# Kernel tuning notes

Hardware: AMD Instinct MI355X
Metric: run time of the kernel (lower is better)

Reference implementation:

```python
import jax, jax.numpy as jnp
import numpy as np

N_NODES = 50000
N_EDGES = 800000
D_FEAT = 64
EDGE_DIM = 64


def setup_inputs() -> dict:
    key = jax.random.key(0)
    k1, k2, k3, k4 = jax.random.split(key, 4)
    node_feats = jax.random.normal(k1, (N_NODES, D_FEAT), dtype=jnp.float32)
    senders = jax.random.randint(k2, (N_EDGES,), 0, N_NODES, dtype=jnp.int32)
    receivers = jax.random.randint(k3, (N_EDGES,), 0, N_NODES, dtype=jnp.int32)
    # Dense(edge_dim) applied to concat([recv, send]) of width 2*D_FEAT
    W = jax.random.normal(k4, (2 * D_FEAT, EDGE_DIM), dtype=jnp.float32) / np.sqrt(2.0 * D_FEAT)
    b = jnp.zeros((EDGE_DIM,), dtype=jnp.float32)
    return {"node_feats": node_feats, "senders": senders, "receivers": receivers, "W": W, "b": b}


def reference(node_feats, senders, receivers, W, b):
    # gather node features at each edge endpoint: [E, D]
    feats_send = node_feats[senders]
    feats_recv = node_feats[receivers]
    # concat(recv, send) -> [E, 2D], Dense + tanh -> [E, edge_dim]
    edge_feats = jnp.concatenate([feats_recv, feats_send], axis=-1)
    return jnp.tanh(edge_feats @ W + b)
```

## Files before the change

### kernel.cpp

```cpp
#include <hip/hip_runtime.h>

#define N_EDGES 800000
#define N_NODES 50000
#define D 64

typedef __attribute__((ext_vector_type(8))) short bf16x8;
typedef __attribute__((ext_vector_type(4))) float f32x4;

__device__ __forceinline__ unsigned short f2bf(float f) {
    unsigned int u = __float_as_uint(f);
    u += 0x7fffu + ((u >> 16) & 1u);
    return (unsigned short)(u >> 16);
}
__device__ __forceinline__ unsigned int pack2(float a, float b) {
    return (unsigned int)f2bf(a) | ((unsigned int)f2bf(b) << 16);
}

__global__ __launch_bounds__(256) void prep(
    const float* __restrict__ nf, const float* __restrict__ W,
    unsigned short* __restrict__ nodes_bf, unsigned short* __restrict__ wfrag)
{
    if (blockIdx.x == gridDim.x - 1) {
#pragma unroll
        for (int i = 0; i < 4; ++i) {
            const int idx = i * 256 + threadIdx.x;
            const int ki = idx >> 8;
            const int nt = (idx >> 6) & 3;
            const int l  = idx & 63;
            const int m  = l & 15, q = l >> 4;
            const int kbase = ki * 32 + q * 8;
            const int n = nt * 16 + m;
            unsigned short* dst = wfrag + idx * 8;
#pragma unroll
            for (int j = 0; j < 8; ++j)
                dst[j] = f2bf(W[(kbase + j) * D + n]);
        }
    } else {
        const long base = ((long)blockIdx.x * 256 + threadIdx.x) * 8;
        if (base < (long)N_NODES * D) {
            const float4 lo = *(const float4*)(nf + base);
            const float4 hi = *(const float4*)(nf + base + 4);
            uint4 p;
            p.x = pack2(lo.x, lo.y);
            p.y = pack2(lo.z, lo.w);
            p.z = pack2(hi.x, hi.y);
            p.w = pack2(hi.z, hi.w);
            *(uint4*)(nodes_bf + base) = p;
        }
    }
}

__global__ __launch_bounds__(256) void edge_mlp(
    const unsigned short* __restrict__ nodes_bf,
    const bf16x8*        __restrict__ wfrag,
    const int*   __restrict__ senders,
    const int*   __restrict__ receivers,
    const float* __restrict__ bias,
    float*       __restrict__ out)
{
    __shared__ bf16x8 lds_b[1024];

#pragma unroll
    for (int i = 0; i < 4; ++i) {
        const int idx = i * 256 + threadIdx.x;
        lds_b[idx] = wfrag[idx];
    }
    __syncthreads();

    const int lane = threadIdx.x & 63;
    const int m    = lane & 15;
    const int q    = lane >> 4;
    const long wid = (long)blockIdx.x * 4 + (threadIdx.x >> 6);
    const long e0  = wid * 64;

    const int rv = receivers[e0 + lane];
    const int sv = senders[e0 + lane];
    int nidx[2][4];
#pragma unroll
    for (int mt = 0; mt < 4; ++mt) {
        nidx[0][mt] = __shfl(rv, mt * 16 + m, 64);
        nidx[1][mt] = __shfl(sv, mt * 16 + m, 64);
    }

    f32x4 acc[4][4];
#pragma unroll
    for (int mt = 0; mt < 4; ++mt)
#pragma unroll
        for (int nt = 0; nt < 4; ++nt)
            acc[mt][nt] = (f32x4)0.0f;

#pragma unroll
    for (int ki = 0; ki < 4; ++ki) {
        const int k0 = ki * 32 + q * 8;

        bf16x8 bfrag[4];
#pragma unroll
        for (int nt = 0; nt < 4; ++nt)
            bfrag[nt] = lds_b[(ki * 4 + nt) * 64 + lane];

        bf16x8 afrag[4];
#pragma unroll
        for (int mt = 0; mt < 4; ++mt) {
            const int node = nidx[ki >> 1][mt];
            afrag[mt] = *(const bf16x8*)(nodes_bf + node * D + (k0 & 63));
        }

#pragma unroll
        for (int mt = 0; mt < 4; ++mt)
#pragma unroll
            for (int nt = 0; nt < 4; ++nt)
                acc[mt][nt] = __builtin_amdgcn_mfma_f32_16x16x32_bf16(
                    afrag[mt], bfrag[nt], acc[mt][nt], 0, 0, 0);
    }

    float bv[4];
#pragma unroll
    for (int nt = 0; nt < 4; ++nt) bv[nt] = bias[nt * 16 + m];

#pragma unroll
    for (int mt = 0; mt < 4; ++mt) {
#pragma unroll
        for (int r = 0; r < 4; ++r) {
            const long row = e0 + mt * 16 + q * 4 + r;
            float* op = out + row * D + m;
#pragma unroll
            for (int nt = 0; nt < 4; ++nt) {
                const float x  = acc[mt][nt][r] + bv[nt];
                const float ax = __builtin_fabsf(x);
                const float t  = __expf(-2.0f * ax);
                float y = (1.0f - t) * __builtin_amdgcn_rcpf(1.0f + t);
                y = __builtin_copysignf(y, x);
                __builtin_nontemporal_store(y, op + nt * 16);
            }
        }
    }
}

extern "C" void kernel_launch(void* const* d_in, const int* in_sizes, int n_in,
                              void* d_out, int out_size, void* d_ws, size_t ws_size,
                              hipStream_t stream) {
    const float* node_feats = (const float*)d_in[0];
    const int*   senders    = (const int*)d_in[1];
    const int*   receivers  = (const int*)d_in[2];
    const float* W          = (const float*)d_in[3];
    const float* bias       = (const float*)d_in[4];
    float*       out        = (float*)d_out;

    unsigned short* nodes_bf = (unsigned short*)d_ws;
    unsigned short* wfrag    = (unsigned short*)((char*)d_ws + (size_t)N_NODES * D * 2);

    const int node_blocks = ((N_NODES * D / 8) + 255) / 256;
    prep<<<node_blocks + 1, 256, 0, stream>>>(node_feats, W, nodes_bf, wfrag);

    const int n_blocks = N_EDGES / 256;
    edge_mlp<<<n_blocks, 256, 0, stream>>>(nodes_bf, (const bf16x8*)wfrag,
                                           senders, receivers, bias, out);
}
```

Measured before the change: 257.2 us.

## Shrink per-wave edge tile to 16 edges and raise occupancy

Each wave now handles 16 edges instead of 64, so its accumulator drops from 16 MFMA tiles to 4. All A-fragment gathers are issued up front, and the grid is four times larger. Launch bounds request 5 blocks per SM so more waves are resident to hide gather latency. In exchange, every block reloads the 16KB weight fragment into LDS for a quarter as many edges, adding LDS-fill and sync overhead per edge.

```diff
diff --git a/kernel.cpp b/kernel.cpp
--- a/kernel.cpp
+++ b/kernel.cpp
@@ -50,7 +50,7 @@
     }
 }
 
-__global__ __launch_bounds__(256) void edge_mlp(
+__global__ __launch_bounds__(256, 5) void edge_mlp(
     const unsigned short* __restrict__ nodes_bf,
     const bf16x8*        __restrict__ wfrag,
     const int*   __restrict__ senders,
@@ -71,46 +71,29 @@
     const int m    = lane & 15;
     const int q    = lane >> 4;
     const long wid = (long)blockIdx.x * 4 + (threadIdx.x >> 6);
-    const long e0  = wid * 64;
+    const long e0  = wid * 16;
 
-    const int rv = receivers[e0 + lane];
-    const int sv = senders[e0 + lane];
-    int nidx[2][4];
+    const int nr = receivers[e0 + m];
+    const int ns = senders[e0 + m];
+
+    const unsigned short* rrow = nodes_bf + (long)nr * D + q * 8;
+    const unsigned short* srow = nodes_bf + (long)ns * D + q * 8;
+    bf16x8 afrag[4];
+    afrag[0] = *(const bf16x8*)(rrow);
+    afrag[1] = *(const bf16x8*)(rrow + 32);
+    afrag[2] = *(const bf16x8*)(srow);
+    afrag[3] = *(const bf16x8*)(srow + 32);
+
+    f32x4 acc[4];
 #pragma unroll
-    for (int mt = 0; mt < 4; ++mt) {
-        nidx[0][mt] = __shfl(rv, mt * 16 + m, 64);
-        nidx[1][mt] = __shfl(sv, mt * 16 + m, 64);
-    }
-
-    f32x4 acc[4][4];
-#pragma unroll
-    for (int mt = 0; mt < 4; ++mt)
-#pragma unroll
-        for (int nt = 0; nt < 4; ++nt)
-            acc[mt][nt] = (f32x4)0.0f;
+    for (int nt = 0; nt < 4; ++nt) acc[nt] = (f32x4)0.0f;
 
 #pragma unroll
     for (int ki = 0; ki < 4; ++ki) {
-        const int k0 = ki * 32 + q * 8;
-
-        bf16x8 bfrag[4];
 #pragma unroll
         for (int nt = 0; nt < 4; ++nt)
-            bfrag[nt] = lds_b[(ki * 4 + nt) * 64 + lane];
-
-        bf16x8 afrag[4];
-#pragma unroll
-        for (int mt = 0; mt < 4; ++mt) {
-            const int node = nidx[ki >> 1][mt];
-            afrag[mt] = *(const bf16x8*)(nodes_bf + node * D + (k0 & 63));
-        }
-
-#pragma unroll
-        for (int mt = 0; mt < 4; ++mt)
-#pragma unroll
-            for (int nt = 0; nt < 4; ++nt)
-                acc[mt][nt] = __builtin_amdgcn_mfma_f32_16x16x32_bf16(
-                    afrag[mt], bfrag[nt], acc[mt][nt], 0, 0, 0);
+            acc[nt] = __builtin_amdgcn_mfma_f32_16x16x32_bf16(
+                afrag[ki], lds_b[(ki * 4 + nt) * 64 + lane], acc[nt], 0, 0, 0);
     }
 
     float bv[4];
@@ -118,20 +101,16 @@
     for (int nt = 0; nt < 4; ++nt) bv[nt] = bias[nt * 16 + m];
 
 #pragma unroll
-    for (int mt = 0; mt < 4; ++mt) {
+    for (int r = 0; r < 4; ++r) {
+        float* op = out + (e0 + q * 4 + r) * D + m;
 #pragma unroll
-        for (int r = 0; r < 4; ++r) {
-            const long row = e0 + mt * 16 + q * 4 + r;
-            float* op = out + row * D + m;
-#pragma unroll
-            for (int nt = 0; nt < 4; ++nt) {
-                const float x  = acc[mt][nt][r] + bv[nt];
-                const float ax = __builtin_fabsf(x);
-                const float t  = __expf(-2.0f * ax);
-                float y = (1.0f - t) * __builtin_amdgcn_rcpf(1.0f + t);
-                y = __builtin_copysignf(y, x);
-                __builtin_nontemporal_store(y, op + nt * 16);
-            }
+        for (int nt = 0; nt < 4; ++nt) {
+            const float x  = acc[nt][r] + bv[nt];
+            const float ax = __builtin_fabsf(x);
+            const float t  = __expf(-2.0f * ax);
+            float y = (1.0f - t) * __builtin_amdgcn_rcpf(1.0f + t);
+            y = __builtin_copysignf(y, x);
+            __builtin_nontemporal_store(y, op + nt * 16);
         }
     }
 }
@@ -152,7 +131,7 @@
     const int node_blocks = ((N_NODES * D / 8) + 255) / 256;
     prep<<<node_blocks + 1, 256, 0, stream>>>(node_feats, W, nodes_bf, wfrag);
 
-    const int n_blocks = N_EDGES / 256;
+    const int n_blocks = N_EDGES / 64;
     edge_mlp<<<n_blocks, 256, 0, stream>>>(nodes_bf, (const bf16x8*)wfrag,
                                            senders, receivers, bias, out);
 }
```

Measured after the change: 260.8 us. Within noise of the previous version (+1.4%).
